# Kernel tuning notes

Measured on AMD Instinct MI355X. Metric: run time of the kernel, lower is better.

The kernel has to match this reference:

```python
import jax, jax.numpy as jnp
import numpy as np

T, B, E, H = 2048, 2, 1024, 16
Dh = E // H


def setup_inputs() -> dict:
    key = jax.random.key(0)
    ks = jax.random.split(key, 5)
    s = 0.02
    query = jax.random.normal(ks[0], (T, B, E), dtype=jnp.float32)
    Wq = jax.random.normal(ks[1], (E, E), dtype=jnp.float32) * s
    Wk = jax.random.normal(ks[2], (E, E), dtype=jnp.float32) * s
    Wv = jax.random.normal(ks[3], (E, E), dtype=jnp.float32) * s
    Wo = jax.random.normal(ks[4], (E, E), dtype=jnp.float32) * s
    bq = jnp.zeros((E,), jnp.float32)
    bk = jnp.zeros((E,), jnp.float32)
    bv = jnp.zeros((E,), jnp.float32)
    bo = jnp.zeros((E,), jnp.float32)
    # additive causal mask: 0 on/below diagonal, -inf above (standard fairseq usage)
    neg = jnp.finfo(jnp.float32).min
    attn_mask = jnp.where(jnp.triu(jnp.ones((T, T), jnp.bool_), k=1), neg, 0.0).astype(jnp.float32)
    return {"query": query, "Wq": Wq, "bq": bq, "Wk": Wk, "bk": bk,
            "Wv": Wv, "bv": bv, "Wo": Wo, "bo": bo, "attn_mask": attn_mask}


def reference(query, Wq, bq, Wk, bk, Wv, bv, Wo, bo, attn_mask):
    t, b, e = query.shape
    scale = Dh ** -0.5
    # self-attention projections (nn.Linear: x @ W.T + b)
    q = (query @ Wq.T + bq) * scale  # [T,B,E]
    k = query @ Wk.T + bk
    v = query @ Wv.T + bv
    # [T, B*H, Dh] -> [B*H, T, Dh]
    q = q.reshape(t, b * H, Dh).transpose(1, 0, 2)
    k = k.reshape(t, b * H, Dh).transpose(1, 0, 2)
    v = v.reshape(t, b * H, Dh).transpose(1, 0, 2)
    # explicit bmm -> softmax -> bmm (materializes [B*H, T, T])
    attn_weights = jnp.einsum('btd,bsd->bts', q, k) + attn_mask[None, :, :]
    attn_probs = jax.nn.softmax(attn_weights, axis=-1)
    attn = jnp.einsum('bts,bsd->btd', attn_probs, v)  # [B*H, T, Dh]
    attn = attn.transpose(1, 0, 2).reshape(t, b, e)  # [T,B,E]
    out = attn @ Wo.T + bo
    return out
```

## Files before the change

kernel.cpp:

```cpp
#include <hip/hip_runtime.h>


typedef __attribute__((ext_vector_type(8))) short   s16x8;
typedef __attribute__((ext_vector_type(4))) float   f32x4;
typedef __attribute__((ext_vector_type(2))) __fp16  f16x2;
typedef __attribute__((ext_vector_type(4))) __fp16  f16x4;

#define MFMA16(a, b, c) __builtin_amdgcn_mfma_f32_16x16x32_bf16((a), (b), (c), 0, 0, 0)
#define MFMApv(a, b, c) __builtin_amdgcn_mfma_f32_16x16x16f16((a), (b), (c), 0, 0, 0)

static __device__ __forceinline__ unsigned short f2bf(float f) {
    unsigned u = __float_as_uint(f);
    unsigned r = u + 0x7fffu + ((u >> 16) & 1u);
    return (unsigned short)(r >> 16);
}

static __device__ __forceinline__ void gl2lds16(const void* g, void* l) {
    __builtin_amdgcn_global_load_lds(
        (const __attribute__((address_space(1))) unsigned int*)g,
        (__attribute__((address_space(3))) unsigned int*)l, 16, 0, 0);
}

__global__ __launch_bounds__(256) void cvt_all(const float* __restrict__ query,
                                               const float* __restrict__ w0,
                                               const float* __restrict__ w1,
                                               const float* __restrict__ w2,
                                               const float* __restrict__ w3,
                                               unsigned short* __restrict__ Xb,
                                               unsigned short* __restrict__ Wcat) {
    const int bx = blockIdx.x;
    if (bx < 4096) {
        const int i = threadIdx.x;
        const float4 f = reinterpret_cast<const float4*>(query + (size_t)bx * 1024)[i];
        ushort4 u;
        u.x = f2bf(f.x); u.y = f2bf(f.y); u.z = f2bf(f.z); u.w = f2bf(f.w);
        const int mrow = (bx & 1) * 2048 + (bx >> 1);
        reinterpret_cast<ushort4*>(Xb + (size_t)mrow * 1024)[i] = u;
    } else {
        const int j   = bx - 4096;
        const int sel = j >> 10;
        const int i   = (j & 1023) * 256 + threadIdx.x;
        const float* src = (sel == 0) ? w0 : (sel == 1) ? w1 : (sel == 2) ? w2 : w3;
        const float4 f = reinterpret_cast<const float4*>(src)[i];
        ushort4 u;
        u.x = f2bf(f.x); u.y = f2bf(f.y); u.z = f2bf(f.z); u.w = f2bf(f.w);
        reinterpret_cast<ushort4*>(Wcat + (size_t)sel * 1048576)[i] = u;
    }
}

__global__ __launch_bounds__(256) void gemm_qkv(const unsigned short* __restrict__ A,
                                                const unsigned short* __restrict__ W,
                                                const float* __restrict__ b0,
                                                const float* __restrict__ b1,
                                                const float* __restrict__ b2,
                                                unsigned short* __restrict__ outQK,
                                                __fp16* __restrict__ outV) {
    __shared__ __align__(16) unsigned short smem[16384];
    unsigned short* Al = smem;
    unsigned short* Bl = smem + 4096;

    const int tid  = threadIdx.x;
    const int w    = tid >> 6;
    const int lane = tid & 63;
    const int quad = lane >> 4;
    const int c    = lane & 15;
    const int wm   = w >> 1;
    const int wn   = w & 1;

    const int m0 = blockIdx.y * 128;
    const int n0 = blockIdx.x * 128;

    f32x4 acc[4][4];
    #pragma unroll
    for (int mi = 0; mi < 4; ++mi)
        #pragma unroll
        for (int ni = 0; ni < 4; ++ni) acc[mi][ni] = (f32x4){0.f, 0.f, 0.f, 0.f};

    const int srow = tid >> 2;
    const int sci  = (tid & 3) ^ ((tid >> 3) & 3);
    const unsigned short* aG = A + (size_t)(m0 + srow) * 1024 + sci * 8;
    const unsigned short* wG = W + (size_t)(n0 + srow) * 1024 + sci * 8;
    const int soff = srow * 32 + (tid & 3) * 8;

    const int swz = (quad ^ ((c >> 1) & 3)) * 8;

    for (int kk = 0; kk < 32; ++kk) {
        const int k0 = kk * 32;
        __syncthreads();
        gl2lds16(aG + k0,             &Al[soff]);
        gl2lds16(aG + k0 + 64 * 1024, &Al[soff + 64 * 32]);
        gl2lds16(wG + k0,             &Bl[soff]);
        gl2lds16(wG + k0 + 64 * 1024, &Bl[soff + 64 * 32]);
        __syncthreads();

        s16x8 af[4], bf[4];
        #pragma unroll
        for (int mi = 0; mi < 4; ++mi)
            af[mi] = *reinterpret_cast<const s16x8*>(&Al[(wm * 64 + mi * 16 + c) * 32 + swz]);
        #pragma unroll
        for (int ni = 0; ni < 4; ++ni)
            bf[ni] = *reinterpret_cast<const s16x8*>(&Bl[(wn * 64 + ni * 16 + c) * 32 + swz]);
        #pragma unroll
        for (int mi = 0; mi < 4; ++mi)
            #pragma unroll
            for (int ni = 0; ni < 4; ++ni)
                acc[mi][ni] = MFMA16(af[mi], bf[ni], acc[mi][ni]);
    }

    const int sel = n0 >> 10;
    if (sel < 2) {
        const float scale = (sel == 0) ? 0.18033688011112042f : 1.0f;
        const float* bias = (sel == 0) ? b0 : b1;
        #pragma unroll
        for (int ni = 0; ni < 4; ++ni) {
            const int n = n0 + wn * 64 + ni * 16 + c;
            const float bval = bias[n & 1023];
            #pragma unroll
            for (int mi = 0; mi < 4; ++mi)
                #pragma unroll
                for (int r = 0; r < 4; ++r) {
                    const int m = m0 + wm * 64 + mi * 16 + quad * 4 + r;
                    outQK[(size_t)m * 2048 + n] = f2bf((acc[mi][ni][r] + bval) * scale);
                }
        }
    } else {
        __syncthreads();
        #pragma unroll
        for (int ni = 0; ni < 4; ++ni) {
            const int n = wn * 64 + ni * 16 + c;
            const float bval = b2[(n0 - 2048) + n];
            #pragma unroll
            for (int mi = 0; mi < 4; ++mi) {
                const int m = wm * 64 + mi * 16 + quad * 4;
                const f16x2 lo = __builtin_amdgcn_cvt_pkrtz(acc[mi][ni][0] + bval,
                                                            acc[mi][ni][1] + bval);
                const f16x2 hi = __builtin_amdgcn_cvt_pkrtz(acc[mi][ni][2] + bval,
                                                            acc[mi][ni][3] + bval);
                uint2 st;
                st.x = __builtin_bit_cast(unsigned int, lo);
                st.y = __builtin_bit_cast(unsigned int, hi);
                const int phys = n * 128 + (((m >> 3) ^ (n & 15)) << 3) + (m & 7);
                *reinterpret_cast<uint2*>(&smem[phys]) = st;
            }
        }
        __syncthreads();
        const int n = tid >> 1;
        const int vcol = (n0 - 2048) + n;
        const int bb = m0 >> 11, tbase = m0 & 2047;
        __fp16* vdst = outV + ((size_t)((bb * 16 + (vcol >> 6)) * 64 + (vcol & 63))) * 2048 + tbase;
        #pragma unroll
        for (int j = 0; j < 8; ++j) {
            const int lc = (tid & 1) * 8 + j;
            const int phys = n * 128 + ((lc ^ (n & 15)) << 3);
            *reinterpret_cast<uint4*>(vdst + lc * 8) =
                *reinterpret_cast<const uint4*>(&smem[phys]);
        }
    }
}

__global__ __launch_bounds__(256) void gemm_out(const unsigned short* __restrict__ A,
                                                const unsigned short* __restrict__ W,
                                                const float* __restrict__ bias,
                                                float* __restrict__ outF) {
    __shared__ __align__(16) unsigned short Al[64 * 32];
    __shared__ __align__(16) unsigned short Bl[128 * 32];

    const int tid  = threadIdx.x;
    const int w    = tid >> 6;
    const int lane = tid & 63;
    const int quad = lane >> 4;
    const int c    = lane & 15;

    const int m0 = blockIdx.y * 64;
    const int n0 = blockIdx.x * 128;

    f32x4 acc[8];
    #pragma unroll
    for (int ni = 0; ni < 8; ++ni) acc[ni] = (f32x4){0.f, 0.f, 0.f, 0.f};

    const int srow = tid >> 2;
    const int sci  = (tid & 3) ^ ((tid >> 3) & 3);
    const unsigned short* aG = A + (size_t)(m0 + srow) * 1024 + sci * 8;
    const unsigned short* wG = W + (size_t)(n0 + srow) * 1024 + sci * 8;
    const int aoff = srow * 32 + (tid & 3) * 8;

    const int swz = (quad ^ ((c >> 1) & 3)) * 8;

    for (int kk = 0; kk < 32; ++kk) {
        const int k0 = kk * 32;
        __syncthreads();
        gl2lds16(aG + k0,             &Al[aoff]);
        gl2lds16(wG + k0,             &Bl[aoff]);
        gl2lds16(wG + k0 + 64 * 1024, &Bl[aoff + 64 * 32]);
        __syncthreads();

        const s16x8 af = *reinterpret_cast<const s16x8*>(&Al[(w * 16 + c) * 32 + swz]);
        #pragma unroll
        for (int ni = 0; ni < 8; ++ni) {
            const s16x8 bf = *reinterpret_cast<const s16x8*>(&Bl[(ni * 16 + c) * 32 + swz]);
            acc[ni] = MFMA16(af, bf, acc[ni]);
        }
    }

    #pragma unroll
    for (int ni = 0; ni < 8; ++ni) {
        const int n = n0 + ni * 16 + c;
        const float bval = bias[n];
        const int m = m0 + w * 16 + quad * 4;
        const int bb = m >> 11, t = m & 2047;
        #pragma unroll
        for (int r = 0; r < 4; ++r)
            outF[(size_t)(2 * (t + r) + bb) * 1024 + n] = acc[ni][r] + bval;
    }
}

__global__ __launch_bounds__(256, 4) void attn_kernel(const unsigned short* __restrict__ QKb,
                                                      const __fp16* __restrict__ Vt,
                                                      unsigned short* __restrict__ Ob) {
    __shared__ unsigned short Kl[2][2][64][32];
    __shared__ __fp16 Vl[2][64][64];

    const int tid  = threadIdx.x;
    const int w    = tid >> 6;
    const int lane = tid & 63;
    const int quad = lane >> 4;
    const int c    = lane & 15;

    const int bh = blockIdx.x, bB = bh >> 4, h = bh & 15;
    const int a  = 31 - (int)blockIdx.y;
    const int t0 = a * 64;
    const int trg = t0 + w * 16;
    const int nIt = a + 1;

    const unsigned short* qp = QKb + (size_t)(bB * 2048 + trg + c) * 2048 + h * 64 + quad * 8;
    const s16x8 aq0 = *reinterpret_cast<const s16x8*>(qp);
    const s16x8 aq1 = *reinterpret_cast<const s16x8*>(qp + 32);

    const int lr4 = lane >> 2, sl4 = lane & 3;
    const unsigned short* kSrc = QKb + (size_t)(bB * 2048 + w * 16 + lr4) * 2048
                                 + 1024 + h * 64 + (sl4 ^ ((lane >> 3) & 3)) * 8;
    const int vr8 = lane >> 3, sl8 = lane & 7;
    const __fp16* vSrcA = Vt + (size_t)(bh * 64 + w * 16 + vr8) * 2048 + (sl8 ^ vr8) * 8;
    const __fp16* vSrcB = vSrcA + (size_t)8 * 2048;

    f32x4 acc[4];
    float l = 0.f;
    #pragma unroll
    for (int dt = 0; dt < 4; ++dt) acc[dt] = (f32x4){0.f, 0.f, 0.f, 0.f};

    const int kswz = (quad ^ ((c >> 1) & 3)) * 8;

    {
        gl2lds16(kSrc,      &Kl[0][0][w * 16 + lr4][sl4 * 8]);
        gl2lds16(kSrc + 32, &Kl[0][1][w * 16 + lr4][sl4 * 8]);
        gl2lds16(vSrcA,     &Vl[0][w * 16 + vr8][sl8 * 8]);
        gl2lds16(vSrcB,     &Vl[0][w * 16 + 8 + vr8][sl8 * 8]);
    }

    for (int it = 0; it < nIt; ++it) {
        const int buf = it & 1;
        __syncthreads();
        if (it + 1 < nIt) {
            const size_t s1 = (size_t)(it + 1) * 64;
            const int nb = buf ^ 1;
            gl2lds16(kSrc + s1 * 2048,      &Kl[nb][0][w * 16 + lr4][sl4 * 8]);
            gl2lds16(kSrc + s1 * 2048 + 32, &Kl[nb][1][w * 16 + lr4][sl4 * 8]);
            gl2lds16(vSrcA + s1,            &Vl[nb][w * 16 + vr8][sl8 * 8]);
            gl2lds16(vSrcB + s1,            &Vl[nb][w * 16 + 8 + vr8][sl8 * 8]);
        }

        s16x8 kf[4][2];
        #pragma unroll
        for (int ns = 0; ns < 4; ++ns) {
            kf[ns][0] = *reinterpret_cast<const s16x8*>(&Kl[buf][0][ns * 16 + c][kswz]);
            kf[ns][1] = *reinterpret_cast<const s16x8*>(&Kl[buf][1][ns * 16 + c][kswz]);
        }
        f16x4 vf[4][4];
        #pragma unroll
        for (int dt = 0; dt < 4; ++dt)
            #pragma unroll
            for (int ch = 0; ch < 4; ++ch) {
                const int phys = ((2 * ch + (quad >> 1)) ^ (c & 7)) * 8 + (quad & 1) * 4;
                vf[dt][ch] = *reinterpret_cast<const f16x4*>(&Vl[buf][dt * 16 + c][phys]);
            }

        const int s0 = it * 64;
        const bool diag = (it == a);
        f32x4 sT[4];
        #pragma unroll
        for (int ns = 0; ns < 4; ++ns) {
            f32x4 z = (f32x4){0.f, 0.f, 0.f, 0.f};
            z = MFMA16(kf[ns][0], aq0, z);
            sT[ns] = MFMA16(kf[ns][1], aq1, z);
        }
        f16x4 pf[4];
        float lp = 0.f;
        #pragma unroll
        for (int ns = 0; ns < 4; ++ns) {
            float pv[4];
            #pragma unroll
            for (int r = 0; r < 4; ++r) pv[r] = exp2f(sT[ns][r]);
            if (diag) {
                const int sb = s0 + ns * 16 + quad * 4;
                const int qg = trg + c;
                #pragma unroll
                for (int r = 0; r < 4; ++r) if (sb + r > qg) pv[r] = 0.f;
            }
            lp += (pv[0] + pv[1]) + (pv[2] + pv[3]);
            const f16x2 lo = __builtin_amdgcn_cvt_pkrtz(pv[0], pv[1]);
            const f16x2 hi = __builtin_amdgcn_cvt_pkrtz(pv[2], pv[3]);
            pf[ns] = __builtin_shufflevector(lo, hi, 0, 1, 2, 3);
        }
        l += lp;
        #pragma unroll
        for (int dt = 0; dt < 4; ++dt)
            #pragma unroll
            for (int ns = 0; ns < 4; ++ns)
                acc[dt] = MFMApv(vf[dt][ns], pf[ns], acc[dt]);
    }

    float lv = l;
    lv += __shfl_xor(lv, 16);
    lv += __shfl_xor(lv, 32);
    const float inv = 1.0f / lv;
    const size_t base = (size_t)(bB * 2048 + trg + c) * 1024 + h * 64;
    #pragma unroll
    for (int dt = 0; dt < 4; ++dt) {
        const unsigned u0 = (unsigned)f2bf(acc[dt][0] * inv)
                          | ((unsigned)f2bf(acc[dt][1] * inv) << 16);
        const unsigned u1 = (unsigned)f2bf(acc[dt][2] * inv)
                          | ((unsigned)f2bf(acc[dt][3] * inv) << 16);
        uint2 st; st.x = u0; st.y = u1;
        *reinterpret_cast<uint2*>(Ob + base + dt * 16 + quad * 4) = st;
    }
}

extern "C" void kernel_launch(void* const* d_in, const int* in_sizes, int n_in,
                              void* d_out, int out_size, void* d_ws, size_t ws_size,
                              hipStream_t stream) {
    const float* query = (const float*)d_in[0];
    const float* Wq    = (const float*)d_in[1];
    const float* bq    = (const float*)d_in[2];
    const float* Wk    = (const float*)d_in[3];
    const float* bk    = (const float*)d_in[4];
    const float* Wv    = (const float*)d_in[5];
    const float* bv    = (const float*)d_in[6];
    const float* Wo    = (const float*)d_in[7];
    const float* bo    = (const float*)d_in[8];

    float* out = (float*)d_out;

    unsigned short* ws    = (unsigned short*)d_ws;
    unsigned short* Xbf   = ws;
    unsigned short* Wcat  = Xbf  + (size_t)4096 * 1024;
    unsigned short* QKb   = Wcat + (size_t)4 * 1024 * 1024;
    __fp16*         Vtw   = (__fp16*)(QKb + (size_t)4096 * 2048);
    unsigned short* attnb = (unsigned short*)(Vtw + (size_t)32 * 64 * 2048);

    cvt_all<<<8192, 256, 0, stream>>>(query, Wq, Wk, Wv, Wo, Xbf, Wcat);

    gemm_qkv<<<dim3(24, 32), 256, 0, stream>>>(Xbf, Wcat, bq, bk, bv, QKb, Vtw);

    attn_kernel<<<dim3(32, 32), 256, 0, stream>>>(QKb, Vtw, attnb);

    gemm_out<<<dim3(8, 64), 256, 0, stream>>>(attnb, Wcat + (size_t)3 * 1024 * 1024,
                                              bo, out);
}
```

Measured before the change: 209.5 us.

## Double GEMM K-tile to 64 and remap blocks for XCD L2 locality

Both GEMM kernels now stage a 64-wide K slice per iteration instead of 32, using an XOR-swizzled 64-column LDS layout. This halves the number of barrier pairs and raises the MFMA work done per sync. All three main kernels also switch to a 1D grid whose block index is remapped so blocks placed on the same XCD share M tiles or heads, aiming for better L2 reuse. The cost is more LDS per block, which could lower occupancy.

```diff
diff --git a/kernel.cpp b/kernel.cpp
--- a/kernel.cpp
+++ b/kernel.cpp
@@ -57,7 +57,7 @@
                                                 __fp16* __restrict__ outV) {
     __shared__ __align__(16) unsigned short smem[16384];
     unsigned short* Al = smem;
-    unsigned short* Bl = smem + 4096;
+    unsigned short* Bl = smem + 8192;
 
     const int tid  = threadIdx.x;
     const int w    = tid >> 6;
@@ -67,8 +67,11 @@
     const int wm   = w >> 1;
     const int wn   = w & 1;
 
-    const int m0 = blockIdx.y * 128;
-    const int n0 = blockIdx.x * 128;
+    const int id   = blockIdx.x;
+    const int xcd  = id & 7;
+    const int slot = id >> 3;
+    const int m0 = (xcd * 4 + (slot & 3)) * 128;
+    const int n0 = (slot >> 2) * 128;
 
     f32x4 acc[4][4];
     #pragma unroll
@@ -76,35 +79,44 @@
         #pragma unroll
         for (int ni = 0; ni < 4; ++ni) acc[mi][ni] = (f32x4){0.f, 0.f, 0.f, 0.f};
 
-    const int srow = tid >> 2;
-    const int sci  = (tid & 3) ^ ((tid >> 3) & 3);
-    const unsigned short* aG = A + (size_t)(m0 + srow) * 1024 + sci * 8;
-    const unsigned short* wG = W + (size_t)(n0 + srow) * 1024 + sci * 8;
-    const int soff = srow * 32 + (tid & 3) * 8;
-
-    const int swz = (quad ^ ((c >> 1) & 3)) * 8;
-
-    for (int kk = 0; kk < 32; ++kk) {
-        const int k0 = kk * 32;
-        __syncthreads();
-        gl2lds16(aG + k0,             &Al[soff]);
-        gl2lds16(aG + k0 + 64 * 1024, &Al[soff + 64 * 32]);
-        gl2lds16(wG + k0,             &Bl[soff]);
-        gl2lds16(wG + k0 + 64 * 1024, &Bl[soff + 64 * 32]);
-        __syncthreads();
-
-        s16x8 af[4], bf[4];
+    const int srow = tid >> 3;
+    const int g    = (tid & 7) ^ (srow & 7);
+    const unsigned short* aG = A + (size_t)(m0 + srow) * 1024 + g * 8;
+    const unsigned short* wG = W + (size_t)(n0 + srow) * 1024 + g * 8;
+    const int loff = tid * 8;
+
+    const int cs = (c & 7);
+
+    for (int kk = 0; kk < 16; ++kk) {
+        const int k0 = kk * 64;
+        __syncthreads();
+        #pragma unroll
+        for (int i = 0; i < 4; ++i) {
+            gl2lds16(aG + k0 + i * 32 * 1024, &Al[loff + i * 2048]);
+            gl2lds16(wG + k0 + i * 32 * 1024, &Bl[loff + i * 2048]);
+        }
+        __syncthreads();
+
+        s16x8 af[4][2], bf[4][2];
+        #pragma unroll
+        for (int mi = 0; mi < 4; ++mi) {
+            const int row = (wm * 64 + mi * 16 + c) * 64;
+            af[mi][0] = *reinterpret_cast<const s16x8*>(&Al[row + ((quad ^ cs) << 3)]);
+            af[mi][1] = *reinterpret_cast<const s16x8*>(&Al[row + (((4 + quad) ^ cs) << 3)]);
+        }
+        #pragma unroll
+        for (int ni = 0; ni < 4; ++ni) {
+            const int row = (wn * 64 + ni * 16 + c) * 64;
+            bf[ni][0] = *reinterpret_cast<const s16x8*>(&Bl[row + ((quad ^ cs) << 3)]);
+            bf[ni][1] = *reinterpret_cast<const s16x8*>(&Bl[row + (((4 + quad) ^ cs) << 3)]);
+        }
         #pragma unroll
         for (int mi = 0; mi < 4; ++mi)
-            af[mi] = *reinterpret_cast<const s16x8*>(&Al[(wm * 64 + mi * 16 + c) * 32 + swz]);
-        #pragma unroll
-        for (int ni = 0; ni < 4; ++ni)
-            bf[ni] = *reinterpret_cast<const s16x8*>(&Bl[(wn * 64 + ni * 16 + c) * 32 + swz]);
-        #pragma unroll
-        for (int mi = 0; mi < 4; ++mi)
-            #pragma unroll
-            for (int ni = 0; ni < 4; ++ni)
-                acc[mi][ni] = MFMA16(af[mi], bf[ni], acc[mi][ni]);
+            #pragma unroll
+            for (int ni = 0; ni < 4; ++ni) {
+                acc[mi][ni] = MFMA16(af[mi][0], bf[ni][0], acc[mi][ni]);
+                acc[mi][ni] = MFMA16(af[mi][1], bf[ni][1], acc[mi][ni]);
+            }
     }
 
     const int sel = n0 >> 10;
@@ -162,8 +174,8 @@
                                                 const unsigned short* __restrict__ W,
                                                 const float* __restrict__ bias,
                                                 float* __restrict__ outF) {
-    __shared__ __align__(16) unsigned short Al[64 * 32];
-    __shared__ __align__(16) unsigned short Bl[128 * 32];
+    __shared__ __align__(16) unsigned short Al[64 * 64];
+    __shared__ __align__(16) unsigned short Bl[128 * 64];
 
     const int tid  = threadIdx.x;
     const int w    = tid >> 6;
@@ -171,34 +183,44 @@
     const int quad = lane >> 4;
     const int c    = lane & 15;
 
-    const int m0 = blockIdx.y * 64;
-    const int n0 = blockIdx.x * 128;
+    const int id   = blockIdx.x;
+    const int xcd  = id & 7;
+    const int slot = id >> 3;
+    const int m0 = (xcd * 8 + (slot & 7)) * 64;
+    const int n0 = (slot >> 3) * 128;
 
     f32x4 acc[8];
     #pragma unroll
     for (int ni = 0; ni < 8; ++ni) acc[ni] = (f32x4){0.f, 0.f, 0.f, 0.f};
 
-    const int srow = tid >> 2;
-    const int sci  = (tid & 3) ^ ((tid >> 3) & 3);
-    const unsigned short* aG = A + (size_t)(m0 + srow) * 1024 + sci * 8;
-    const unsigned short* wG = W + (size_t)(n0 + srow) * 1024 + sci * 8;
-    const int aoff = srow * 32 + (tid & 3) * 8;
-
-    const int swz = (quad ^ ((c >> 1) & 3)) * 8;
-
-    for (int kk = 0; kk < 32; ++kk) {
-        const int k0 = kk * 32;
-        __syncthreads();
-        gl2lds16(aG + k0,             &Al[aoff]);
-        gl2lds16(wG + k0,             &Bl[aoff]);
-        gl2lds16(wG + k0 + 64 * 1024, &Bl[aoff + 64 * 32]);
-        __syncthreads();
-
-        const s16x8 af = *reinterpret_cast<const s16x8*>(&Al[(w * 16 + c) * 32 + swz]);
+    const int srow = tid >> 3;
+    const int g    = (tid & 7) ^ (srow & 7);
+    const unsigned short* aG = A + (size_t)(m0 + srow) * 1024 + g * 8;
+    const unsigned short* wG = W + (size_t)(n0 + srow) * 1024 + g * 8;
+    const int loff = tid * 8;
+
+    const int cs = (c & 7);
+
+    for (int kk = 0; kk < 16; ++kk) {
+        const int k0 = kk * 64;
+        __syncthreads();
+        gl2lds16(aG + k0,             &Al[loff]);
+        gl2lds16(aG + k0 + 32 * 1024, &Al[loff + 2048]);
+        #pragma unroll
+        for (int i = 0; i < 4; ++i)
+            gl2lds16(wG + k0 + i * 32 * 1024, &Bl[loff + i * 2048]);
+        __syncthreads();
+
+        const int arow = (w * 16 + c) * 64;
+        const s16x8 af0 = *reinterpret_cast<const s16x8*>(&Al[arow + ((quad ^ cs) << 3)]);
+        const s16x8 af1 = *reinterpret_cast<const s16x8*>(&Al[arow + (((4 + quad) ^ cs) << 3)]);
         #pragma unroll
         for (int ni = 0; ni < 8; ++ni) {
-            const s16x8 bf = *reinterpret_cast<const s16x8*>(&Bl[(ni * 16 + c) * 32 + swz]);
-            acc[ni] = MFMA16(af, bf, acc[ni]);
+            const int brow = (ni * 16 + c) * 64;
+            const s16x8 bf0 = *reinterpret_cast<const s16x8*>(&Bl[brow + ((quad ^ cs) << 3)]);
+            const s16x8 bf1 = *reinterpret_cast<const s16x8*>(&Bl[brow + (((4 + quad) ^ cs) << 3)]);
+            acc[ni] = MFMA16(af0, bf0, acc[ni]);
+            acc[ni] = MFMA16(af1, bf1, acc[ni]);
         }
     }
 
@@ -226,8 +248,10 @@
     const int quad = lane >> 4;
     const int c    = lane & 15;
 
-    const int bh = blockIdx.x, bB = bh >> 4, h = bh & 15;
-    const int a  = 31 - (int)blockIdx.y;
+    const int id = blockIdx.x;
+    const int bh = (id & 7) * 4 + ((id >> 3) & 3);
+    const int a  = 31 - (id >> 5);
+    const int bB = bh >> 4, h = bh & 15;
     const int t0 = a * 64;
     const int trg = t0 + w * 16;
     const int nIt = a + 1;
@@ -359,10 +383,10 @@
 
     cvt_all<<<8192, 256, 0, stream>>>(query, Wq, Wk, Wv, Wo, Xbf, Wcat);
 
-    gemm_qkv<<<dim3(24, 32), 256, 0, stream>>>(Xbf, Wcat, bq, bk, bv, QKb, Vtw);
-
-    attn_kernel<<<dim3(32, 32), 256, 0, stream>>>(QKb, Vtw, attnb);
-
-    gemm_out<<<dim3(8, 64), 256, 0, stream>>>(attnb, Wcat + (size_t)3 * 1024 * 1024,
-                                              bo, out);
-}
+    gemm_qkv<<<768, 256, 0, stream>>>(Xbf, Wcat, bq, bk, bv, QKb, Vtw);
+
+    attn_kernel<<<1024, 256, 0, stream>>>(QKb, Vtw, attnb);
+
+    gemm_out<<<512, 256, 0, stream>>>(attnb, Wcat + (size_t)3 * 1024 * 1024,
+                                      bo, out);
+}
```

Result: faster. 199.7 us (-4.6%).
